# Optimization experiments

Measured on AMD Instinct MI355X. Metric: run time of the kernel, lower is better.

Reference implementation:

```python
import jax, jax.numpy as jnp
import numpy as np

B, CTX, DIMS, HEAD = 8, 4096, 1024, 16
HD = DIMS // HEAD
EPS = 1e-5
THRESH = 0.01   # self.threshold.item()
FACTOR = 0.1    # self.factor.item()
MAX_IT = 3


def setup_inputs() -> dict:
    key = jax.random.key(0)
    ks = jax.random.split(key, 9)
    w = lambda k, shp: jax.random.normal(k, shp, jnp.float32) * 0.02
    return {
        "x": jax.random.normal(ks[0], (B, CTX, DIMS), jnp.float32),
        "qw": w(ks[1], (DIMS, DIMS)), "qb": jnp.zeros((DIMS,), jnp.float32),
        "kw": w(ks[2], (DIMS, DIMS)),  # k linear has bias=False
        "vw": w(ks[3], (DIMS, DIMS)), "vb": jnp.zeros((DIMS,), jnp.float32),
        "ow": w(ks[4], (DIMS, DIMS)), "ob": jnp.zeros((DIMS,), jnp.float32),
        "lna_w": jnp.ones((DIMS,), jnp.float32),
        "lnb_w": jnp.ones((DIMS,), jnp.float32),
        "lnc_w": jnp.ones((HD,), jnp.float32),
        "lnd_w": jnp.ones((HD,), jnp.float32),
        "lqw": w(ks[5], (HD, HD)), "lqb": jnp.zeros((HD,), jnp.float32),
        "lkw": w(ks[6], (HD, HD)), "lkb": jnp.zeros((HD,), jnp.float32),
        "lvw": w(ks[7], (HD, HD)), "lvb": jnp.zeros((HD,), jnp.float32),
    }


def _ln(x, w):
    # torch LayerNorm with bias=False (biased variance)
    m = jnp.mean(x, axis=-1, keepdims=True)
    v = jnp.mean((x - m) ** 2, axis=-1, keepdims=True)
    return (x - m) * jax.lax.rsqrt(v + EPS) * w


def reference(x, qw, qb, kw, vw, vb, ow, ob, lna_w, lnb_w, lnc_w, lnd_w,
              lqw, lqb, lkw, lkb, lvw, lvb):
    b, ctx, dims = x.shape
    q = _ln(x, lna_w) @ qw.T + qb
    xb = _ln(x, lnb_w)
    k = xb @ kw.T
    v = xb @ vw.T + vb
    split = lambda t: t.reshape(b, ctx, HEAD, HD).transpose(0, 2, 1, 3)  # [b,h,s,d]
    query, key_t, value = split(q), split(k), split(v)

    # Faithful to source bug: eff_span = min(seq, qcur.size(1)=head, key.size(1)=head)
    eff = min(ctx, HEAD)

    # key/value side of the inner loop is iteration-invariant -> compute once
    kn = _ln(key_t[:, :, :eff, :] @ lkw.T + lkb, lnd_w)
    vi = value[:, :, :eff, :] @ lvw.T + lvb
    scale = 1.0 / np.sqrt(HD)

    def step(qcur):
        qn = _ln(qcur[:, :, :eff, :] @ lqw.T + lqb, lnc_w)
        logits = jnp.einsum('bhqd,bhkd->bhqk', qn, kn) * scale
        attn = jax.nn.softmax(logits, axis=-1) @ vi  # is_causal=False (mask is None)
        return jnp.zeros_like(qcur).at[:, :, :eff, :].set(attn)

    prev = jnp.zeros_like(query)
    attn_out = jnp.zeros_like(query)
    qcur = query
    done = jnp.asarray(False)
    for it in range(MAX_IT):
        iter_out = step(qcur)
        diff = jnp.mean(jnp.abs(iter_out - prev))
        brk = (diff < THRESH + FACTOR * diff) & jnp.asarray(it > 0) & (~done)
        attn_out = jnp.where(done, attn_out, iter_out)
        prev = jnp.where(done, prev, iter_out)
        qcur = jnp.where(done | brk, qcur, qcur + iter_out)
        done = done | brk

    out = attn_out.transpose(0, 2, 1, 3).reshape(b, ctx, dims)
    return out @ ow.T + ob
```

## Files before the change

### kernel.cpp

```cpp
#include <hip/hip_runtime.h>

typedef unsigned short u16;
typedef __attribute__((ext_vector_type(8))) short short8;
typedef __attribute__((ext_vector_type(4))) float f32x4;

#define LSTR 68
#define ASTR 1032

__device__ __forceinline__ u16 f2bf(float f){
  union { float f; unsigned int i; } v; v.f = f;
  unsigned int x = v.i;
  return (u16)((x + 0x7FFFu + ((x >> 16) & 1u)) >> 16);
}

__device__ __forceinline__ short8 cvt8(const float* __restrict__ p){
  float4 a = *(const float4*)p;
  float4 b = *(const float4*)(p + 4);
  short8 r;
  r[0]=(short)f2bf(a.x); r[1]=(short)f2bf(a.y); r[2]=(short)f2bf(a.z); r[3]=(short)f2bf(a.w);
  r[4]=(short)f2bf(b.x); r[5]=(short)f2bf(b.y); r[6]=(short)f2bf(b.z); r[7]=(short)f2bf(b.w);
  return r;
}

__global__ __launch_bounds__(256) void k_lnproj(const float* __restrict__ x,
    const float* __restrict__ lna, const float* __restrict__ lnb,
    const float* __restrict__ qw, const float* __restrict__ qb,
    const float* __restrict__ kw, const float* __restrict__ vw,
    const float* __restrict__ vb, float* __restrict__ qkv)
{
  __shared__ u16 Aa[16*ASTR];
  __shared__ u16 Ab[16*ASTR];

  int tid = threadIdx.x, wave = tid>>6, lane = tid&63;
  int blk = blockIdx.x;
  int mt  = blk / 48;

  int r = tid >> 4, l16 = tid & 15;
  const float* xr = x + ((size_t)mt*4096 + r)*1024;
  float4 vv[16];
  float sum = 0.f, sq = 0.f;
  #pragma unroll
  for (int j=0;j<16;j++){
    vv[j] = *(const float4*)(xr + (j*16 + l16)*4);
    sum += vv[j].x+vv[j].y+vv[j].z+vv[j].w;
    sq  += vv[j].x*vv[j].x + vv[j].y*vv[j].y + vv[j].z*vv[j].z + vv[j].w*vv[j].w;
  }
  #pragma unroll
  for (int m=1;m<16;m<<=1){ sum += __shfl_xor(sum,m); sq += __shfl_xor(sq,m); }
  float mn  = sum * (1.f/1024.f);
  float var = sq  * (1.f/1024.f) - mn*mn;
  float rs  = rsqrtf(fmaxf(var, 0.f) + 1e-5f);
  #pragma unroll
  for (int j=0;j<16;j++){
    int c = (j*16 + l16)*4;
    float4 wa = *(const float4*)(lna + c);
    float4 wb = *(const float4*)(lnb + c);
    float n0=(vv[j].x-mn)*rs, n1=(vv[j].y-mn)*rs, n2=(vv[j].z-mn)*rs, n3=(vv[j].w-mn)*rs;
    ushort4 oa, obv;
    oa.x =f2bf(n0*wa.x); oa.y =f2bf(n1*wa.y); oa.z =f2bf(n2*wa.z); oa.w =f2bf(n3*wa.w);
    obv.x=f2bf(n0*wb.x); obv.y=f2bf(n1*wb.y); obv.z=f2bf(n2*wb.z); obv.w=f2bf(n3*wb.w);
    *(ushort4*)(Aa + r*ASTR + c) = oa;
    *(ushort4*)(Ab + r*ASTR + c) = obv;
  }
  __syncthreads();

  int tile = blk*4 + wave;
  int nt = tile % 192, mat = nt >> 6, nct = nt & 63;
  const u16*   Al = (mat==0) ? Aa : Ab;
  const float* W  = (mat==0) ? qw : ((mat==1) ? kw : vw);
  int m_lane = lane & 15, quad = lane >> 4;
  const u16*   ap = Al + m_lane*ASTR + quad*8;
  const float* bp = W + (size_t)(nct*16 + m_lane)*1024 + quad*8;
  f32x4 acc = {0.f,0.f,0.f,0.f};
  #pragma unroll 4
  for (int k0=0;k0<1024;k0+=32){
    short8 af = *(const short8*)(ap + k0);
    short8 bf = cvt8(bp + k0);
    acc = __builtin_amdgcn_mfma_f32_16x16x32_bf16(af, bf, acc, 0, 0, 0);
  }
  int n = nct*16 + m_lane;
  float bias = 0.f;
  if (mat==0) bias = qb[n];
  else if (mat==2) bias = vb[n];
  float* outp = qkv + (size_t)mat*131072;
  #pragma unroll
  for (int i=0;i<4;i++){
    int row = mt*16 + quad*4 + i;
    outp[(size_t)row*1024 + n] = acc[i] + bias;
  }
}

__device__ __forceinline__ void mm4(const float* __restrict__ X, const float* __restrict__ W,
                                    const float* __restrict__ bias, int r, int cg, float out4[4])
{
  const float* xrow = X + r*LSTR;
  #pragma unroll
  for (int i=0;i<4;i++){
    int o = cg*4+i;
    const float* wrow = W + o*LSTR;
    float acc = bias[o];
    #pragma unroll
    for (int d=0; d<64; d+=4){
      float4 w4 = *(const float4*)(wrow + d);
      float4 x4 = *(const float4*)(xrow + d);
      acc += x4.x*w4.x + x4.y*w4.y + x4.z*w4.z + x4.w*w4.w;
    }
    out4[i] = acc;
  }
}

__device__ __forceinline__ void ln4(float v[4], const float* __restrict__ lnw, int cg)
{
  float s = v[0]+v[1]+v[2]+v[3];
  float q = v[0]*v[0]+v[1]*v[1]+v[2]*v[2]+v[3]*v[3];
  #pragma unroll
  for (int m=1;m<16;m<<=1){ s += __shfl_xor(s,m); q += __shfl_xor(q,m); }
  float mn  = s * (1.f/64.f);
  float var = q * (1.f/64.f) - mn*mn;
  float rs  = rsqrtf(fmaxf(var,0.f) + 1e-5f);
  #pragma unroll
  for (int i=0;i<4;i++) v[i] = (v[i]-mn)*rs*lnw[cg*4+i];
}

__device__ __forceinline__ void attn_iter(const float* __restrict__ qsrc,
    const float* __restrict__ wq, const float* __restrict__ lqb, const float* __restrict__ lnc,
    float* __restrict__ qns, float* __restrict__ ps,
    const float* __restrict__ kks, const float* __restrict__ vis,
    int r, int cg, float a4[4])
{
  int c0 = cg*4;
  float qn4[4];
  mm4(qsrc, wq, lqb, r, cg, qn4);
  ln4(qn4, lnc, cg);
  #pragma unroll
  for (int i=0;i<4;i++) qns[r*LSTR+c0+i] = qn4[i];
  __syncthreads();
  float acc = 0.f;
  #pragma unroll
  for (int d=0;d<64;d+=4){
    float4 a = *(const float4*)(qns + r*LSTR + d);
    float4 b = *(const float4*)(kks + cg*LSTR + d);
    acc += a.x*b.x + a.y*b.y + a.z*b.z + a.w*b.w;
  }
  acc *= 0.125f;
  float mx = acc;
  #pragma unroll
  for (int m=1;m<16;m<<=1) mx = fmaxf(mx, __shfl_xor(mx,m));
  float e = __expf(acc - mx);
  float sm = e;
  #pragma unroll
  for (int m=1;m<16;m<<=1) sm += __shfl_xor(sm,m);
  ps[r*17+cg] = e / sm;
  __syncthreads();
  #pragma unroll
  for (int i=0;i<4;i++){
    int o = c0+i; float s = 0.f;
    #pragma unroll
    for (int c=0;c<16;c++) s += ps[r*17+c]*vis[c*LSTR+o];
    a4[i] = s;
  }
}

__global__ __launch_bounds__(256) void k_attn(const float* __restrict__ qkv,
    const float* __restrict__ lnc, const float* __restrict__ lnd,
    const float* __restrict__ lqw, const float* __restrict__ lqb,
    const float* __restrict__ lkw, const float* __restrict__ lkb,
    const float* __restrict__ lvw, const float* __restrict__ lvb,
    u16* __restrict__ attn)
{
  __shared__ float qs[16*LSTR], ks[16*LSTR], vs[16*LSTR];
  __shared__ float kks[16*LSTR], vis[16*LSTR], qns[16*LSTR], qcs[16*LSTR];
  __shared__ float ps[16*17];
  __shared__ float wq[64*LSTR], wk[64*LSTR], wv[64*LSTR];
  __shared__ float sb[5*64];

  int tid = threadIdx.x, bh = blockIdx.x;
  int b = bh>>4, h = bh&15;
  int r = tid>>4, cg = tid&15, c0 = cg*4;

  for (int i = tid; i < 1024; i += 256){
    int o = i >> 4, d = (i & 15)*4;
    *(float4*)(wq + o*LSTR + d) = *(const float4*)(lqw + i*4);
    *(float4*)(wk + o*LSTR + d) = *(const float4*)(lkw + i*4);
    *(float4*)(wv + o*LSTR + d) = *(const float4*)(lvw + i*4);
  }
  if (tid < 64){
    sb[tid]       = lqb[tid];
    sb[64  + tid] = lkb[tid];
    sb[128 + tid] = lvb[tid];
    sb[192 + tid] = lnc[tid];
    sb[256 + tid] = lnd[tid];
  }
  size_t base = (size_t)(b*16 + r)*1024 + h*64 + c0;
  float4 fq = *(const float4*)(qkv + base);
  float4 fk = *(const float4*)(qkv + 131072 + base);
  float4 fv = *(const float4*)(qkv + 262144 + base);
  float q4[4] = {fq.x, fq.y, fq.z, fq.w};
  #pragma unroll
  for (int i=0;i<4;i++) qs[r*LSTR+c0+i] = q4[i];
  *(float4*)(ks + r*LSTR + c0) = fk;
  *(float4*)(vs + r*LSTR + c0) = fv;
  __syncthreads();

  float kk4[4]; mm4(ks, wk, sb+64, r, cg, kk4); ln4(kk4, sb+256, cg);
  float vi4[4]; mm4(vs, wv, sb+128, r, cg, vi4);
  #pragma unroll
  for (int i=0;i<4;i++){ kks[r*LSTR+c0+i] = kk4[i]; vis[r*LSTR+c0+i] = vi4[i]; }
  __syncthreads();

  float a4[4];
  attn_iter(qs, wq, sb+0, sb+192, qns, ps, kks, vis, r, cg, a4);
  #pragma unroll
  for (int i=0;i<4;i++) qcs[r*LSTR+c0+i] = q4[i] + a4[i];
  __syncthreads();
  attn_iter(qcs, wq, sb+0, sb+192, qns, ps, kks, vis, r, cg, a4);

  ushort4 ov;
  ov.x=f2bf(a4[0]); ov.y=f2bf(a4[1]); ov.z=f2bf(a4[2]); ov.w=f2bf(a4[3]);
  *(ushort4*)(attn + (size_t)(b*16 + r)*1024 + h*64 + c0) = ov;
}

__global__ __launch_bounds__(256) void k_fillproj(const u16* __restrict__ attn,
    const float* __restrict__ ow, const float* __restrict__ ob, float* __restrict__ out)
{
  int tid = threadIdx.x;
  if (blockIdx.x < 32768){
    int row = blockIdx.x;
    if ((row & 4095) < 16) return;
    *(float4*)(out + (size_t)row*1024 + tid*4) = *(const float4*)(ob + tid*4);
    return;
  }
  int wave = tid>>6, lane = tid&63;
  int tile = (blockIdx.x - 32768)*4 + wave;
  int mt = tile >> 6, nt = tile & 63;
  int m_lane = lane & 15, quad = lane >> 4;
  const u16*   ap = attn + (size_t)(mt*16 + m_lane)*1024 + quad*8;
  const float* bp = ow   + (size_t)(nt*16 + m_lane)*1024 + quad*8;
  f32x4 acc = {0.f,0.f,0.f,0.f};
  #pragma unroll 4
  for (int k0=0;k0<1024;k0+=32){
    short8 af = *(const short8*)(ap + k0);
    short8 bf = cvt8(bp + k0);
    acc = __builtin_amdgcn_mfma_f32_16x16x32_bf16(af, bf, acc, 0, 0, 0);
  }
  int n = nt*16 + m_lane;
  float bias = ob[n];
  #pragma unroll
  for (int i=0;i<4;i++){
    int s = quad*4 + i;
    out[((size_t)mt*4096 + s)*1024 + n] = acc[i] + bias;
  }
}

extern "C" void kernel_launch(void* const* d_in, const int* in_sizes, int n_in,
                              void* d_out, int out_size, void* d_ws, size_t ws_size,
                              hipStream_t stream)
{
  const float* x    = (const float*)d_in[0];
  const float* qw   = (const float*)d_in[1];
  const float* qb   = (const float*)d_in[2];
  const float* kw   = (const float*)d_in[3];
  const float* vw   = (const float*)d_in[4];
  const float* vb   = (const float*)d_in[5];
  const float* ow   = (const float*)d_in[6];
  const float* ob   = (const float*)d_in[7];
  const float* lna  = (const float*)d_in[8];
  const float* lnb  = (const float*)d_in[9];
  const float* lnc  = (const float*)d_in[10];
  const float* lnd  = (const float*)d_in[11];
  const float* lqw  = (const float*)d_in[12];
  const float* lqb  = (const float*)d_in[13];
  const float* lkw  = (const float*)d_in[14];
  const float* lkb  = (const float*)d_in[15];
  const float* lvw  = (const float*)d_in[16];
  const float* lvb  = (const float*)d_in[17];

  char* ws = (char*)d_ws;
  float* qkv  = (float*)(ws);
  u16*   attn = (u16*)(ws + 1572864);
  float* out  = (float*)d_out;

  k_lnproj  <<<  384, 256, 0, stream>>>(x, lna, lnb, qw, qb, kw, vw, vb, qkv);
  k_attn    <<<  128, 256, 0, stream>>>(qkv, lnc, lnd, lqw, lqb, lkw, lkb, lvw, lvb, attn);
  k_fillproj<<<32896, 256, 0, stream>>>(attn, ow, ob, out);
}
```

Measured before the change: 283.9 us.

## Fuse LN+QKV projection into attention kernel and overlap bias fill

Merges the LayerNorm/QKV projection kernel into the per-(batch,head) attention kernel. Each block now computes only its head's 64 Q/K/V columns into shared memory, which removes the qkv workspace round trip and one launch. The LN weights are folded into the weight conversion so only one normalized tile is needed. The large bias-fill of output rows is moved into extra grid-stride blocks of the same launch, and the output projection runs as a small separate kernel. The cost is that the projection work now runs on only 128 blocks, and the LN scale is applied to weights on every block.

```diff
diff --git a/kernel.cpp b/kernel.cpp
--- a/kernel.cpp
+++ b/kernel.cpp
@@ -6,6 +6,7 @@
 
 #define LSTR 68
 #define ASTR 1032
+#define FILLB 2048
 
 __device__ __forceinline__ u16 f2bf(float f){
   union { float f; unsigned int i; } v; v.f = f;
@@ -22,81 +23,13 @@
   return r;
 }
 
-__global__ __launch_bounds__(256) void k_lnproj(const float* __restrict__ x,
-    const float* __restrict__ lna, const float* __restrict__ lnb,
-    const float* __restrict__ qw, const float* __restrict__ qb,
-    const float* __restrict__ kw, const float* __restrict__ vw,
-    const float* __restrict__ vb, float* __restrict__ qkv)
-{
-  __shared__ u16 Aa[16*ASTR];
-  __shared__ u16 Ab[16*ASTR];
-
-  int tid = threadIdx.x, wave = tid>>6, lane = tid&63;
-  int blk = blockIdx.x;
-  int mt  = blk / 48;
-
-  int r = tid >> 4, l16 = tid & 15;
-  const float* xr = x + ((size_t)mt*4096 + r)*1024;
-  float4 vv[16];
-  float sum = 0.f, sq = 0.f;
-  #pragma unroll
-  for (int j=0;j<16;j++){
-    vv[j] = *(const float4*)(xr + (j*16 + l16)*4);
-    sum += vv[j].x+vv[j].y+vv[j].z+vv[j].w;
-    sq  += vv[j].x*vv[j].x + vv[j].y*vv[j].y + vv[j].z*vv[j].z + vv[j].w*vv[j].w;
-  }
-  #pragma unroll
-  for (int m=1;m<16;m<<=1){ sum += __shfl_xor(sum,m); sq += __shfl_xor(sq,m); }
-  float mn  = sum * (1.f/1024.f);
-  float var = sq  * (1.f/1024.f) - mn*mn;
-  float rs  = rsqrtf(fmaxf(var, 0.f) + 1e-5f);
-  #pragma unroll
-  for (int j=0;j<16;j++){
-    int c = (j*16 + l16)*4;
-    float4 wa = *(const float4*)(lna + c);
-    float4 wb = *(const float4*)(lnb + c);
-    float n0=(vv[j].x-mn)*rs, n1=(vv[j].y-mn)*rs, n2=(vv[j].z-mn)*rs, n3=(vv[j].w-mn)*rs;
-    ushort4 oa, obv;
-    oa.x =f2bf(n0*wa.x); oa.y =f2bf(n1*wa.y); oa.z =f2bf(n2*wa.z); oa.w =f2bf(n3*wa.w);
-    obv.x=f2bf(n0*wb.x); obv.y=f2bf(n1*wb.y); obv.z=f2bf(n2*wb.z); obv.w=f2bf(n3*wb.w);
-    *(ushort4*)(Aa + r*ASTR + c) = oa;
-    *(ushort4*)(Ab + r*ASTR + c) = obv;
-  }
-  __syncthreads();
-
-  int tile = blk*4 + wave;
-  int nt = tile % 192, mat = nt >> 6, nct = nt & 63;
-  const u16*   Al = (mat==0) ? Aa : Ab;
-  const float* W  = (mat==0) ? qw : ((mat==1) ? kw : vw);
-  int m_lane = lane & 15, quad = lane >> 4;
-  const u16*   ap = Al + m_lane*ASTR + quad*8;
-  const float* bp = W + (size_t)(nct*16 + m_lane)*1024 + quad*8;
-  f32x4 acc = {0.f,0.f,0.f,0.f};
-  #pragma unroll 4
-  for (int k0=0;k0<1024;k0+=32){
-    short8 af = *(const short8*)(ap + k0);
-    short8 bf = cvt8(bp + k0);
-    acc = __builtin_amdgcn_mfma_f32_16x16x32_bf16(af, bf, acc, 0, 0, 0);
-  }
-  int n = nct*16 + m_lane;
-  float bias = 0.f;
-  if (mat==0) bias = qb[n];
-  else if (mat==2) bias = vb[n];
-  float* outp = qkv + (size_t)mat*131072;
-  #pragma unroll
-  for (int i=0;i<4;i++){
-    int row = mt*16 + quad*4 + i;
-    outp[(size_t)row*1024 + n] = acc[i] + bias;
-  }
-}
-
 __device__ __forceinline__ void mm4(const float* __restrict__ X, const float* __restrict__ W,
                                     const float* __restrict__ bias, int r, int cg, float out4[4])
 {
   const float* xrow = X + r*LSTR;
   #pragma unroll
   for (int i=0;i<4;i++){
-    int o = cg*4+i;
+    int o = i*16 + cg;
     const float* wrow = W + o*LSTR;
     float acc = bias[o];
     #pragma unroll
@@ -119,7 +52,7 @@
   float var = q * (1.f/64.f) - mn*mn;
   float rs  = rsqrtf(fmaxf(var,0.f) + 1e-5f);
   #pragma unroll
-  for (int i=0;i<4;i++) v[i] = (v[i]-mn)*rs*lnw[cg*4+i];
+  for (int i=0;i<4;i++) v[i] = (v[i]-mn)*rs*lnw[i*16+cg];
 }
 
 __device__ __forceinline__ void attn_iter(const float* __restrict__ qsrc,
@@ -128,19 +61,18 @@
     const float* __restrict__ kks, const float* __restrict__ vis,
     int r, int cg, float a4[4])
 {
-  int c0 = cg*4;
   float qn4[4];
   mm4(qsrc, wq, lqb, r, cg, qn4);
   ln4(qn4, lnc, cg);
   #pragma unroll
-  for (int i=0;i<4;i++) qns[r*LSTR+c0+i] = qn4[i];
+  for (int i=0;i<4;i++) qns[r*LSTR + i*16 + cg] = qn4[i];
   __syncthreads();
   float acc = 0.f;
   #pragma unroll
   for (int d=0;d<64;d+=4){
-    float4 a = *(const float4*)(qns + r*LSTR + d);
-    float4 b = *(const float4*)(kks + cg*LSTR + d);
-    acc += a.x*b.x + a.y*b.y + a.z*b.z + a.w*b.w;
+    float4 a  = *(const float4*)(qns + r*LSTR + d);
+    float4 bv = *(const float4*)(kks + cg*LSTR + d);
+    acc += a.x*bv.x + a.y*bv.y + a.z*bv.z + a.w*bv.w;
   }
   acc *= 0.125f;
   float mx = acc;
@@ -152,6 +84,7 @@
   for (int m=1;m<16;m<<=1) sm += __shfl_xor(sm,m);
   ps[r*17+cg] = e / sm;
   __syncthreads();
+  int c0 = cg*4;
   #pragma unroll
   for (int i=0;i<4;i++){
     int o = c0+i; float s = 0.f;
@@ -161,28 +94,48 @@
   }
 }
 
-__global__ __launch_bounds__(256) void k_attn(const float* __restrict__ qkv,
+__global__ __launch_bounds__(256) void k_main(const float* __restrict__ x,
+    const float* __restrict__ lna, const float* __restrict__ lnb,
+    const float* __restrict__ qw, const float* __restrict__ qb,
+    const float* __restrict__ kw, const float* __restrict__ vw,
+    const float* __restrict__ vb,
     const float* __restrict__ lnc, const float* __restrict__ lnd,
     const float* __restrict__ lqw, const float* __restrict__ lqb,
     const float* __restrict__ lkw, const float* __restrict__ lkb,
     const float* __restrict__ lvw, const float* __restrict__ lvb,
-    u16* __restrict__ attn)
-{
+    const float* __restrict__ ob, u16* __restrict__ attn, float* __restrict__ out)
+{
+  __shared__ u16 An[16*ASTR];
+  __shared__ float wqs[64*LSTR], wks[64*LSTR], wvs[64*LSTR];
   __shared__ float qs[16*LSTR], ks[16*LSTR], vs[16*LSTR];
   __shared__ float kks[16*LSTR], vis[16*LSTR], qns[16*LSTR], qcs[16*LSTR];
   __shared__ float ps[16*17];
-  __shared__ float wq[64*LSTR], wk[64*LSTR], wv[64*LSTR];
   __shared__ float sb[5*64];
 
-  int tid = threadIdx.x, bh = blockIdx.x;
-  int b = bh>>4, h = bh&15;
-  int r = tid>>4, cg = tid&15, c0 = cg*4;
+  int tid = threadIdx.x;
+
+  if (blockIdx.x >= 128){
+    int fb = blockIdx.x - 128;
+    const int SPAN = 4080*256;
+    const int TOT  = 8*SPAN;
+    float4 val = *(const float4*)(ob + tid*4);
+    for (int idx = fb*256 + tid; idx < TOT; idx += FILLB*256){
+      int b   = idx / SPAN;
+      int rem = idx - b*SPAN;
+      *((float4*)out + ((size_t)b*1048576 + 4096 + rem)) = val;
+    }
+    return;
+  }
+
+  int b = blockIdx.x >> 4, h = blockIdx.x & 15;
+  int wave = tid>>6, lane = tid&63;
+  int r = tid >> 4, l16 = tid & 15;
 
   for (int i = tid; i < 1024; i += 256){
     int o = i >> 4, d = (i & 15)*4;
-    *(float4*)(wq + o*LSTR + d) = *(const float4*)(lqw + i*4);
-    *(float4*)(wk + o*LSTR + d) = *(const float4*)(lkw + i*4);
-    *(float4*)(wv + o*LSTR + d) = *(const float4*)(lvw + i*4);
+    *(float4*)(wqs + o*LSTR + d) = *(const float4*)(lqw + i*4);
+    *(float4*)(wks + o*LSTR + d) = *(const float4*)(lkw + i*4);
+    *(float4*)(wvs + o*LSTR + d) = *(const float4*)(lvw + i*4);
   }
   if (tid < 64){
     sb[tid]       = lqb[tid];
@@ -191,47 +144,89 @@
     sb[192 + tid] = lnc[tid];
     sb[256 + tid] = lnd[tid];
   }
-  size_t base = (size_t)(b*16 + r)*1024 + h*64 + c0;
-  float4 fq = *(const float4*)(qkv + base);
-  float4 fk = *(const float4*)(qkv + 131072 + base);
-  float4 fv = *(const float4*)(qkv + 262144 + base);
-  float q4[4] = {fq.x, fq.y, fq.z, fq.w};
-  #pragma unroll
-  for (int i=0;i<4;i++) qs[r*LSTR+c0+i] = q4[i];
-  *(float4*)(ks + r*LSTR + c0) = fk;
-  *(float4*)(vs + r*LSTR + c0) = fv;
-  __syncthreads();
-
-  float kk4[4]; mm4(ks, wk, sb+64, r, cg, kk4); ln4(kk4, sb+256, cg);
-  float vi4[4]; mm4(vs, wv, sb+128, r, cg, vi4);
-  #pragma unroll
-  for (int i=0;i<4;i++){ kks[r*LSTR+c0+i] = kk4[i]; vis[r*LSTR+c0+i] = vi4[i]; }
+
+  const float* xr = x + ((size_t)b*4096 + r)*1024;
+  float4 vv[16];
+  float sum = 0.f, sq = 0.f;
+  #pragma unroll
+  for (int j=0;j<16;j++){
+    vv[j] = *(const float4*)(xr + (j*16 + l16)*4);
+    sum += vv[j].x+vv[j].y+vv[j].z+vv[j].w;
+    sq  += vv[j].x*vv[j].x + vv[j].y*vv[j].y + vv[j].z*vv[j].z + vv[j].w*vv[j].w;
+  }
+  #pragma unroll
+  for (int m=1;m<16;m<<=1){ sum += __shfl_xor(sum,m); sq += __shfl_xor(sq,m); }
+  float mn  = sum * (1.f/1024.f);
+  float var = sq  * (1.f/1024.f) - mn*mn;
+  float rs  = rsqrtf(fmaxf(var, 0.f) + 1e-5f);
+  #pragma unroll
+  for (int j=0;j<16;j++){
+    int c = (j*16 + l16)*4;
+    ushort4 oa;
+    oa.x = f2bf((vv[j].x-mn)*rs); oa.y = f2bf((vv[j].y-mn)*rs);
+    oa.z = f2bf((vv[j].z-mn)*rs); oa.w = f2bf((vv[j].w-mn)*rs);
+    *(ushort4*)(An + r*ASTR + c) = oa;
+  }
+  __syncthreads();
+
+  int m_lane = lane & 15, quad = lane >> 4;
+  #pragma unroll
+  for (int tt=0; tt<3; ++tt){
+    int t = wave*3 + tt;
+    int mat = t >> 2, ncl = t & 3;
+    const float* W  = (mat==0) ? qw  : ((mat==1) ? kw  : vw);
+    const float* sc = (mat==0) ? lna : lnb;
+    int ncol = h*64 + ncl*16 + m_lane;
+    const u16*   ap = An + m_lane*ASTR + quad*8;
+    const float* bp = W + (size_t)ncol*1024 + quad*8;
+    const float* sp = sc + quad*8;
+    f32x4 acc = {0.f,0.f,0.f,0.f};
+    #pragma unroll 4
+    for (int k0=0;k0<1024;k0+=32){
+      short8 af = *(const short8*)(ap + k0);
+      float4 w0 = *(const float4*)(bp + k0);
+      float4 w1 = *(const float4*)(bp + k0 + 4);
+      float4 s0 = *(const float4*)(sp + k0);
+      float4 s1 = *(const float4*)(sp + k0 + 4);
+      short8 bf;
+      bf[0]=(short)f2bf(w0.x*s0.x); bf[1]=(short)f2bf(w0.y*s0.y);
+      bf[2]=(short)f2bf(w0.z*s0.z); bf[3]=(short)f2bf(w0.w*s0.w);
+      bf[4]=(short)f2bf(w1.x*s1.x); bf[5]=(short)f2bf(w1.y*s1.y);
+      bf[6]=(short)f2bf(w1.z*s1.z); bf[7]=(short)f2bf(w1.w*s1.w);
+      acc = __builtin_amdgcn_mfma_f32_16x16x32_bf16(af, bf, acc, 0, 0, 0);
+    }
+    float bias = (mat==0) ? qb[ncol] : ((mat==2) ? vb[ncol] : 0.f);
+    float* dst = (mat==0) ? qs : ((mat==1) ? ks : vs);
+    #pragma unroll
+    for (int i=0;i<4;i++)
+      dst[(quad*4+i)*LSTR + ncl*16 + m_lane] = acc[i] + bias;
+  }
+  __syncthreads();
+
+  int cg = tid & 15, c0 = cg*4;
+  float kk4[4]; mm4(ks, wks, sb+64, r, cg, kk4); ln4(kk4, sb+256, cg);
+  float vi4[4]; mm4(vs, wvs, sb+128, r, cg, vi4);
+  #pragma unroll
+  for (int i=0;i<4;i++){ kks[r*LSTR + i*16 + cg] = kk4[i]; vis[r*LSTR + i*16 + cg] = vi4[i]; }
   __syncthreads();
 
   float a4[4];
-  attn_iter(qs, wq, sb+0, sb+192, qns, ps, kks, vis, r, cg, a4);
-  #pragma unroll
-  for (int i=0;i<4;i++) qcs[r*LSTR+c0+i] = q4[i] + a4[i];
-  __syncthreads();
-  attn_iter(qcs, wq, sb+0, sb+192, qns, ps, kks, vis, r, cg, a4);
+  attn_iter(qs, wqs, sb+0, sb+192, qns, ps, kks, vis, r, cg, a4);
+  #pragma unroll
+  for (int i=0;i<4;i++) qcs[r*LSTR + c0 + i] = qs[r*LSTR + c0 + i] + a4[i];
+  __syncthreads();
+  attn_iter(qcs, wqs, sb+0, sb+192, qns, ps, kks, vis, r, cg, a4);
 
   ushort4 ov;
   ov.x=f2bf(a4[0]); ov.y=f2bf(a4[1]); ov.z=f2bf(a4[2]); ov.w=f2bf(a4[3]);
   *(ushort4*)(attn + (size_t)(b*16 + r)*1024 + h*64 + c0) = ov;
 }
 
-__global__ __launch_bounds__(256) void k_fillproj(const u16* __restrict__ attn,
+__global__ __launch_bounds__(128) void k_oproj(const u16* __restrict__ attn,
     const float* __restrict__ ow, const float* __restrict__ ob, float* __restrict__ out)
 {
-  int tid = threadIdx.x;
-  if (blockIdx.x < 32768){
-    int row = blockIdx.x;
-    if ((row & 4095) < 16) return;
-    *(float4*)(out + (size_t)row*1024 + tid*4) = *(const float4*)(ob + tid*4);
-    return;
-  }
-  int wave = tid>>6, lane = tid&63;
-  int tile = (blockIdx.x - 32768)*4 + wave;
+  int tid = threadIdx.x, wave = tid>>6, lane = tid&63;
+  int tile = blockIdx.x*2 + wave;
   int mt = tile >> 6, nt = tile & 63;
   int m_lane = lane & 15, quad = lane >> 4;
   const u16*   ap = attn + (size_t)(mt*16 + m_lane)*1024 + quad*8;
@@ -275,12 +270,11 @@
   const float* lvw  = (const float*)d_in[16];
   const float* lvb  = (const float*)d_in[17];
 
-  char* ws = (char*)d_ws;
-  float* qkv  = (float*)(ws);
-  u16*   attn = (u16*)(ws + 1572864);
-  float* out  = (float*)d_out;
-
-  k_lnproj  <<<  384, 256, 0, stream>>>(x, lna, lnb, qw, qb, kw, vw, vb, qkv);
-  k_attn    <<<  128, 256, 0, stream>>>(qkv, lnc, lnd, lqw, lqb, lkw, lkb, lvw, lvb, attn);
-  k_fillproj<<<32896, 256, 0, stream>>>(attn, ow, ob, out);
-}
+  u16* attn = (u16*)d_ws;
+  float* out = (float*)d_out;
+
+  k_main <<<128 + FILLB, 256, 0, stream>>>(x, lna, lnb, qw, qb, kw, vw, vb,
+                                           lnc, lnd, lqw, lqb, lkw, lkb, lvw, lvb,
+                                           ob, attn, out);
+  k_oproj<<<256, 128, 0, stream>>>(attn, ow, ob, out);
+}
```

After: 282.4 us. About the same (-0.5%).
